# Kernel tuning notes

Hardware: AMD Instinct MI355X
Metric: run time of the kernel (lower is better)

The kernel has to match this reference:

```python
import jax, jax.numpy as jnp
import numpy as np

VERTEX_W = 1.0
SMOOTH_W = 0.1
SYM_W = 0.05
CHAMFER_W = 0.1

B, N = 4, 8192  # N points per cloud, flat dim = N*3


def setup_inputs() -> dict:
    key = jax.random.key(0)
    k1, k2 = jax.random.split(key)
    pred = jax.random.normal(k1, (B, N * 3), dtype=jnp.float32)
    targ = jax.random.normal(k2, (B, N * 3), dtype=jnp.float32)
    return {"pred_vertices": pred, "target_vertices": targ}


def _chamfer(x, y):
    # x: [B,N,3], y: [B,M,3]; euclidean cdist via matmul expansion
    x2 = jnp.sum(x * x, axis=-1)  # [B,N]
    y2 = jnp.sum(y * y, axis=-1)  # [B,M]
    xy = jnp.einsum('bnd,bmd->bnm', x, y)  # [B,N,M]
    d2 = x2[:, :, None] + y2[None if False else slice(None), None, :] - 2.0 * xy
    d = jnp.sqrt(jnp.maximum(d2, 0.0))
    return jnp.mean(jnp.min(d, axis=2)) + jnp.mean(jnp.min(d, axis=1))


def reference(pred_vertices, target_vertices):
    b = pred_vertices.shape[0]
    pv = pred_vertices.reshape(b, -1, 3)
    tv = target_vertices.reshape(b, -1, 3)

    # vertex MSE (on flat tensors, same as mse on reshaped)
    vertex_loss = jnp.mean((pred_vertices - target_vertices) ** 2)

    # smoothness: mean L2 norm of consecutive vertex diffs
    diff = pv[:, 1:, :] - pv[:, :-1, :]
    smoothness_loss = jnp.mean(jnp.linalg.norm(diff, axis=2))

    # symmetry: N is even in this config
    mid = pv.shape[1] // 2
    left = pv[:, :mid, :]
    right = jnp.flip(pv[:, mid:, :], axis=1)
    right = right.at[:, :, 0].multiply(-1.0)
    symmetry_loss = jnp.mean((left - right) ** 2)

    chamfer_loss = _chamfer(pv, tv)

    total = (VERTEX_W * vertex_loss + SMOOTH_W * smoothness_loss
             + SYM_W * symmetry_loss + CHAMFER_W * chamfer_loss)
    return total
```

## Files before the change

kernel.cpp:

```cpp
#include <hip/hip_runtime.h>
#include <hip/hip_bf16.h>


#define B_ 4
#define N_ 8192
#define MID_ (N_ / 2)
#define CNT_OFF 1536
#define RP_OFF 1664
#define PM_OFF 4096
#define PACK_OFF (PM_OFF + 4 * 2 * B_ * N_)
#define PACK_STRIDE (B_ * N_ * 16)

typedef short short8 __attribute__((ext_vector_type(8)));
typedef float f32x16 __attribute__((ext_vector_type(16)));

__global__ void AdvancedLoss3D_1881195675843_kernel() {}

__device__ __forceinline__ void async16(void* lds, const void* g) {
    __builtin_amdgcn_global_load_lds(
        (const __attribute__((address_space(1))) unsigned int*)g,
        (__attribute__((address_space(3))) unsigned int*)lds,
        16, 0, 0);
}

__device__ inline unsigned short bfu(float x) {
    union { __hip_bfloat16 b; unsigned short u; } c;
    c.b = __float2bfloat16(x);
    return c.u;
}
__device__ inline float bff(unsigned short u) {
    union { __hip_bfloat16 b; unsigned short u; } c;
    c.u = u;
    return __bfloat162float(c.b);
}

__device__ inline void enc(float x, float y, float z,
                           unsigned short* A, unsigned short* Bv) {
    float n2 = fmaf(x, x, fmaf(y, y, z * z));
    unsigned short hx = bfu(x), hy = bfu(y), hz = bfu(z);
    float fx = bff(hx), fy = bff(hy), fz = bff(hz);
    unsigned short lx = bfu(x - fx), ly = bfu(y - fy), lz = bfu(z - fz);
    unsigned short mx = bfu(-2.f * fx), my = bfu(-2.f * fy), mz = bfu(-2.f * fz);
    unsigned short nx = bfu(-2.f * bff(lx)), ny = bfu(-2.f * bff(ly)),
                   nz = bfu(-2.f * bff(lz));
    unsigned short n2h = bfu(n2);
    unsigned short n2l = bfu(n2 - bff(n2h));
    unsigned short one = bfu(1.0f);
    A[0] = mx; A[1] = my; A[2] = mz;
    A[3] = mx; A[4] = my; A[5] = mz;
    A[6] = nx; A[7] = ny; A[8] = nz;
    A[9] = n2h; A[10] = n2l; A[11] = one; A[12] = one;
    A[13] = A[14] = A[15] = 0;
    Bv[0] = hx; Bv[1] = hy; Bv[2] = hz;
    Bv[3] = lx; Bv[4] = ly; Bv[5] = lz;
    Bv[6] = hx; Bv[7] = hy; Bv[8] = hz;
    Bv[9] = one; Bv[10] = one; Bv[11] = n2h; Bv[12] = n2l;
    Bv[13] = Bv[14] = Bv[15] = 0;
}

__global__ __launch_bounds__(64) void prep_aux(const float* __restrict__ pred,
                                               const float* __restrict__ targ,
                                               float* __restrict__ ws) {
    int idx = blockIdx.x * 64 + threadIdx.x;
    int b = idx >> 13;
    int i = idx & (N_ - 1);
    const float* p = pred + (size_t)idx * 3;
    const float* t = targ + (size_t)idx * 3;
    float px = p[0], py = p[1], pz = p[2];
    float tx = t[0], ty = t[1], tz = t[2];

    if (idx == 0) ((unsigned int*)ws)[CNT_OFF] = 0u;

    unsigned short* pk = (unsigned short*)(ws + PACK_OFF);
    {
        union U { unsigned short s[16]; uint4 q[2]; } ua, ub, uc, ud;
        enc(px, py, pz, ua.s, ub.s);
        enc(tx, ty, tz, uc.s, ud.s);
        uint4* ap = (uint4*)(pk + (size_t)idx * 16);
        ap[0] = ua.q[0]; ap[1] = ua.q[1];
        uint4* bp = (uint4*)(pk + PACK_STRIDE + (size_t)idx * 16);
        bp[0] = ub.q[0]; bp[1] = ub.q[1];
        uint4* at = (uint4*)(pk + 2 * PACK_STRIDE + (size_t)idx * 16);
        at[0] = uc.q[0]; at[1] = uc.q[1];
        uint4* bt = (uint4*)(pk + 3 * PACK_STRIDE + (size_t)idx * 16);
        bt[0] = ud.q[0]; bt[1] = ud.q[1];
    }

    float dx = px - tx, dy = py - ty, dz = pz - tz;
    float dv = dx * dx + dy * dy + dz * dz;

    float sm = 0.f;
    if (i < N_ - 1) {
        float ex = p[3] - px, ey = p[4] - py, ez = p[5] - pz;
        sm = sqrtf(ex * ex + ey * ey + ez * ez);
    }

    float sy = 0.f;
    if (i < MID_) {
        const float* r = pred + ((size_t)(b * N_ + (N_ - 1 - i))) * 3;
        float ax = px + r[0];
        float ay = py - r[1];
        float az = pz - r[2];
        sy = ax * ax + ay * ay + az * az;
    }

    for (int off = 32; off; off >>= 1) {
        dv += __shfl_down(dv, off, 64);
        sm += __shfl_down(sm, off, 64);
        sy += __shfl_down(sy, off, 64);
    }
    if (threadIdx.x == 0) {
        ws[3 * blockIdx.x + 0] = dv;
        ws[3 * blockIdx.x + 1] = sm;
        ws[3 * blockIdx.x + 2] = sy;
    }
}

__global__ __launch_bounds__(256) void chamfer_mfma(const unsigned short* __restrict__ packs,
                                                    float* __restrict__ pm) {
    int bid = blockIdx.x;
    int chunk = bid & 31;
    int rgb = bid >> 5;
    int dir = chunk >> 4;
    int b   = (chunk >> 2) & 3;
    int cc  = chunk & 3;
    int w   = threadIdx.x >> 6;
    int l   = threadIdx.x & 63;
    int lr  = l & 31;
    int kh  = l >> 5;

    const unsigned short* Ap = packs + (dir ? 2 : 0) * PACK_STRIDE;
    const unsigned short* Bp = packs + (dir ? 1 : 3) * PACK_STRIDE;

    int rowbase = (rgb * 4 + w) * 64;
    const unsigned short* abase = Ap + ((size_t)(b * N_ + rowbase + lr)) * 16 + kh * 8;
    short8 af0 = *(const short8*)abase;
    short8 af1 = *(const short8*)(abase + 32 * 16);

    float rmin0[16], rmin1[16];
#pragma unroll
    for (int j = 0; j < 16; j++) { rmin0[j] = 3.4e38f; rmin1[j] = 3.4e38f; }

    __shared__ __align__(16) unsigned char smem[32768];
    const unsigned short* bchunk = Bp + (size_t)(b * N_ + cc * 2048) * 16;

    const f32x16 zero = {0.f, 0.f, 0.f, 0.f, 0.f, 0.f, 0.f, 0.f,
                         0.f, 0.f, 0.f, 0.f, 0.f, 0.f, 0.f, 0.f};

#define STAGE(buf, g)                                                        \
    do {                                                                     \
        int _t0 = (g) * 8 + 2 * w;         \
        async16(smem + (buf) * 8192 + 2 * w * 1024,                          \
                bchunk + (size_t)_t0 * 512 + l * 8);                         \
        async16(smem + (buf) * 8192 + (2 * w + 1) * 1024,                    \
                bchunk + (size_t)(_t0 + 1) * 512 + l * 8);                   \
    } while (0)

    STAGE(0, 0);
    __syncthreads();
    for (int g = 0; g < 8; ++g) {
        if (g + 1 < 8) STAGE((g + 1) & 1, g + 1);
        const unsigned char* bb = smem + (g & 1) * 8192;
#pragma unroll
        for (int tp = 0; tp < 8; tp += 2) {
            short8 bE = *(const short8*)(bb + tp * 1024 + lr * 32 + kh * 16);
            short8 bO = *(const short8*)(bb + (tp + 1) * 1024 + lr * 32 + kh * 16);
            f32x16 aE = __builtin_amdgcn_mfma_f32_32x32x16_bf16(af0, bE, zero, 0, 0, 0);
            f32x16 aO = __builtin_amdgcn_mfma_f32_32x32x16_bf16(af0, bO, zero, 0, 0, 0);
#pragma unroll
            for (int j = 0; j < 16; j++)
                rmin0[j] = fminf(fminf(rmin0[j], aE[j]), aO[j]);
            aE = __builtin_amdgcn_mfma_f32_32x32x16_bf16(af1, bE, zero, 0, 0, 0);
            aO = __builtin_amdgcn_mfma_f32_32x32x16_bf16(af1, bO, zero, 0, 0, 0);
#pragma unroll
            for (int j = 0; j < 16; j++)
                rmin1[j] = fminf(fminf(rmin1[j], aE[j]), aO[j]);
        }
        __syncthreads();
    }
#undef STAGE

    float (*sred)[64][32] = (float (*)[64][32])smem;
#pragma unroll
    for (int j = 0; j < 16; j++) {
        int r0 = (j & 3) + 8 * (j >> 2) + 4 * kh;
        sred[w][r0][(lr + r0) & 31] = rmin0[j];
        int r1 = 32 + r0;
        sred[w][r1][(lr + r1) & 31] = rmin1[j];
    }
    __syncthreads();
    float v = 3.4e38f;
#pragma unroll
    for (int c = 0; c < 32; c++)
        v = fminf(v, sred[w][l][(c + l) & 31]);
    pm[(size_t)cc * 65536 + dir * 32768 + b * N_ + rowbase + l] = v;
}

__global__ __launch_bounds__(256) void reduce_compose(const float* __restrict__ pm,
                                                      float* __restrict__ ws,
                                                      unsigned int* __restrict__ out) {
    int bid = blockIdx.x, tid = threadIdx.x;
    int idx = bid * 256 + tid;
    float v = 3.4e38f;
#pragma unroll
    for (int s = 0; s < 4; s++)
        v = fminf(v, pm[(size_t)s * 65536 + idx]);
    float d = sqrtf(fmaxf(v, 0.f));
    for (int off = 32; off; off >>= 1) d += __shfl_down(d, off, 64);
    __shared__ float red[4];
    __shared__ int is_last;
    int lane = tid & 63, w = tid >> 6;
    if (lane == 0) red[w] = d;
    __syncthreads();
    if (tid == 0) {
        ws[RP_OFF + bid] = red[0] + red[1] + red[2] + red[3];
        __threadfence();
        unsigned old = atomicAdd((unsigned int*)ws + CNT_OFF, 1u);
        is_last = (old == 255u);
    }
    __syncthreads();
    if (!is_last) return;

    if (tid == 0) __threadfence();
    __syncthreads();
    float rp = ws[RP_OFF + tid];
    float cr = (tid < 128) ? rp : 0.f;
    float cc = (tid < 128) ? 0.f : rp;
    float dv = ws[3 * tid]     + ws[3 * (tid + 256)];
    float sm = ws[3 * tid + 1] + ws[3 * (tid + 256) + 1];
    float sy = ws[3 * tid + 2] + ws[3 * (tid + 256) + 2];
    for (int off = 32; off; off >>= 1) {
        dv += __shfl_down(dv, off, 64);
        sm += __shfl_down(sm, off, 64);
        sy += __shfl_down(sy, off, 64);
        cr += __shfl_down(cr, off, 64);
        cc += __shfl_down(cc, off, 64);
    }
    __shared__ float red5[5][4];
    if (lane == 0) { red5[0][w] = dv; red5[1][w] = sm; red5[2][w] = sy;
                     red5[3][w] = cr; red5[4][w] = cc; }
    __syncthreads();
    if (tid == 0) {
        float S[5];
#pragma unroll
        for (int q = 0; q < 5; q++)
            S[q] = red5[q][0] + red5[q][1] + red5[q][2] + red5[q][3];
        float vertex = S[0] / (float)(B_ * N_ * 3);
        float smooth = S[1] / (float)(B_ * (N_ - 1));
        float sym    = S[2] / (float)(B_ * MID_ * 3);
        float cham   = (S[3] + S[4]) / (float)(B_ * N_);
        float total  = vertex + 0.1f * smooth + 0.05f * sym + 0.1f * cham;
        union { __hip_bfloat16 b; unsigned short u; } cv;
        cv.b = __float2bfloat16(total);
        out[0] = ((unsigned int)cv.u << 16) | (unsigned int)cv.u;
    }
}

extern "C" void kernel_launch(void* const* d_in, const int* in_sizes, int n_in,
                              void* d_out, int out_size, void* d_ws, size_t ws_size,
                              hipStream_t stream) {
    (void)in_sizes; (void)n_in; (void)out_size; (void)ws_size;
    const float* pred = (const float*)d_in[0];
    const float* targ = (const float*)d_in[1];
    float* wsf = (float*)d_ws;

    prep_aux<<<dim3(512), dim3(64), 0, stream>>>(pred, targ, wsf);
    chamfer_mfma<<<dim3(1024), dim3(256), 0, stream>>>(
        (const unsigned short*)(wsf + PACK_OFF), wsf + PM_OFF);
    reduce_compose<<<dim3(256), dim3(256), 0, stream>>>(
        wsf + PM_OFF, wsf, (unsigned int*)d_out);
}
```

Baseline: 91.48 us.

## Give each wave 128 rows and load the whole B chunk into LDS once

Each wave now holds four A fragments (128 rows) instead of two, so every B tile read from LDS feeds four MFMA pairs instead of two. The double-buffered staging loop is replaced by a single async load of the full 2048-column B chunk (64 KB of LDS) followed by one barrier. The grid is halved to 512 blocks, and launch bounds request 2 blocks per CU. In exchange there are more accumulator registers, a larger LDS footprint that limits occupancy, no overlap between the load and the compute, and fewer blocks to fill the GPU.

```diff
diff --git a/kernel.cpp b/kernel.cpp
--- a/kernel.cpp
+++ b/kernel.cpp
@@ -116,8 +116,8 @@
     }
 }
 
-__global__ __launch_bounds__(256) void chamfer_mfma(const unsigned short* __restrict__ packs,
-                                                    float* __restrict__ pm) {
+__global__ __launch_bounds__(256, 2) void chamfer_mfma(const unsigned short* __restrict__ packs,
+                                                       float* __restrict__ pm) {
     int bid = blockIdx.x;
     int chunk = bid & 31;
     int rgb = bid >> 5;
@@ -132,68 +132,67 @@
     const unsigned short* Ap = packs + (dir ? 2 : 0) * PACK_STRIDE;
     const unsigned short* Bp = packs + (dir ? 1 : 3) * PACK_STRIDE;
 
-    int rowbase = (rgb * 4 + w) * 64;
+    int rowbase = (rgb * 4 + w) * 128;
     const unsigned short* abase = Ap + ((size_t)(b * N_ + rowbase + lr)) * 16 + kh * 8;
-    short8 af0 = *(const short8*)abase;
-    short8 af1 = *(const short8*)(abase + 32 * 16);
-
-    float rmin0[16], rmin1[16];
-#pragma unroll
-    for (int j = 0; j < 16; j++) { rmin0[j] = 3.4e38f; rmin1[j] = 3.4e38f; }
-
-    __shared__ __align__(16) unsigned char smem[32768];
+    short8 af[4];
+#pragma unroll
+    for (int i = 0; i < 4; i++)
+        af[i] = *(const short8*)(abase + i * 32 * 16);
+
+    float rmin[4][16];
+#pragma unroll
+    for (int i = 0; i < 4; i++)
+#pragma unroll
+        for (int j = 0; j < 16; j++) rmin[i][j] = 3.4e38f;
+
+    __shared__ __align__(16) unsigned char smem[65536];
     const unsigned short* bchunk = Bp + (size_t)(b * N_ + cc * 2048) * 16;
+    {
+        const unsigned short* src = bchunk + (size_t)(lr * 16 + kh * 8);
+#pragma unroll
+        for (int t = 0; t < 16; t++) {
+            int tile = w * 16 + t;
+            async16(smem + (size_t)tile * 1024, src + (size_t)tile * 512);
+        }
+    }
+    __syncthreads();
 
     const f32x16 zero = {0.f, 0.f, 0.f, 0.f, 0.f, 0.f, 0.f, 0.f,
                          0.f, 0.f, 0.f, 0.f, 0.f, 0.f, 0.f, 0.f};
-
-#define STAGE(buf, g)                                                        \
-    do {                                                                     \
-        int _t0 = (g) * 8 + 2 * w;         \
-        async16(smem + (buf) * 8192 + 2 * w * 1024,                          \
-                bchunk + (size_t)_t0 * 512 + l * 8);                         \
-        async16(smem + (buf) * 8192 + (2 * w + 1) * 1024,                    \
-                bchunk + (size_t)(_t0 + 1) * 512 + l * 8);                   \
-    } while (0)
-
-    STAGE(0, 0);
-    __syncthreads();
-    for (int g = 0; g < 8; ++g) {
-        if (g + 1 < 8) STAGE((g + 1) & 1, g + 1);
-        const unsigned char* bb = smem + (g & 1) * 8192;
-#pragma unroll
-        for (int tp = 0; tp < 8; tp += 2) {
-            short8 bE = *(const short8*)(bb + tp * 1024 + lr * 32 + kh * 16);
-            short8 bO = *(const short8*)(bb + (tp + 1) * 1024 + lr * 32 + kh * 16);
-            f32x16 aE = __builtin_amdgcn_mfma_f32_32x32x16_bf16(af0, bE, zero, 0, 0, 0);
-            f32x16 aO = __builtin_amdgcn_mfma_f32_32x32x16_bf16(af0, bO, zero, 0, 0, 0);
+    const unsigned char* bl = smem + kh * 512 + lr * 16;
+    for (int t = 0; t < 64; t += 2) {
+        short8 bE = *(const short8*)(bl + (size_t)t * 1024);
+        short8 bO = *(const short8*)(bl + (size_t)(t + 1) * 1024);
+#pragma unroll
+        for (int i = 0; i < 4; i++) {
+            f32x16 aE = __builtin_amdgcn_mfma_f32_32x32x16_bf16(af[i], bE, zero, 0, 0, 0);
+            f32x16 aO = __builtin_amdgcn_mfma_f32_32x32x16_bf16(af[i], bO, zero, 0, 0, 0);
 #pragma unroll
             for (int j = 0; j < 16; j++)
-                rmin0[j] = fminf(fminf(rmin0[j], aE[j]), aO[j]);
-            aE = __builtin_amdgcn_mfma_f32_32x32x16_bf16(af1, bE, zero, 0, 0, 0);
-            aO = __builtin_amdgcn_mfma_f32_32x32x16_bf16(af1, bO, zero, 0, 0, 0);
-#pragma unroll
-            for (int j = 0; j < 16; j++)
-                rmin1[j] = fminf(fminf(rmin1[j], aE[j]), aO[j]);
+                rmin[i][j] = fminf(fminf(rmin[i][j], aE[j]), aO[j]);
         }
-        __syncthreads();
-    }
-#undef STAGE
-
-    float (*sred)[64][32] = (float (*)[64][32])smem;
-#pragma unroll
-    for (int j = 0; j < 16; j++) {
-        int r0 = (j & 3) + 8 * (j >> 2) + 4 * kh;
-        sred[w][r0][(lr + r0) & 31] = rmin0[j];
-        int r1 = 32 + r0;
-        sred[w][r1][(lr + r1) & 31] = rmin1[j];
-    }
-    __syncthreads();
-    float v = 3.4e38f;
-#pragma unroll
-    for (int c = 0; c < 32; c++)
-        v = fminf(v, sred[w][l][(c + l) & 31]);
-    pm[(size_t)cc * 65536 + dir * 32768 + b * N_ + rowbase + l] = v;
+    }
+    __syncthreads();
+
+    float (*sred)[128][32] = (float (*)[128][32])smem;
+#pragma unroll
+    for (int i = 0; i < 4; i++)
+#pragma unroll
+        for (int j = 0; j < 16; j++) {
+            int r = i * 32 + (j & 3) + 8 * (j >> 2) + 4 * kh;
+            sred[w][r][(lr + r) & 31] = rmin[i][j];
+        }
+    __syncthreads();
+    float* orow = pm + (size_t)cc * 65536 + dir * 32768 + b * N_ + rowbase;
+#pragma unroll
+    for (int rr = 0; rr < 128; rr += 64) {
+        int r = rr + l;
+        float v = 3.4e38f;
+#pragma unroll
+        for (int c = 0; c < 32; c++)
+            v = fminf(v, sred[w][r][(c + r) & 31]);
+        orow[r] = v;
+    }
 }
 
 __global__ __launch_bounds__(256) void reduce_compose(const float* __restrict__ pm,
@@ -265,7 +264,7 @@
     float* wsf = (float*)d_ws;
 
     prep_aux<<<dim3(512), dim3(64), 0, stream>>>(pred, targ, wsf);
-    chamfer_mfma<<<dim3(1024), dim3(256), 0, stream>>>(
+    chamfer_mfma<<<dim3(512), dim3(256), 0, stream>>>(
         (const unsigned short*)(wsf + PACK_OFF), wsf + PM_OFF);
     reduce_compose<<<dim3(256), dim3(256), 0, stream>>>(
         wsf + PM_OFF, wsf, (unsigned int*)d_out);
```

New measurement: 82.42 us. 9.9% less time.
